# Kernel optimization log

Measured on AMD Instinct MI355X. Metric: run time of the kernel, lower is better.

The kernel has to match this reference:

```python
import jax, jax.numpy as jnp
import numpy as np

# ---------------- static model configuration (mirrors NeuroNN.__init__) -------------
N = 2000
RATIO = 0.8
N_E = int(N * RATIO)
N_I = N - N_E
NMAX = 60          # Euler fixed-point steps (Nmax in Euler2fixedpt)
NAVG = 15          # trailing steps averaged for convergence metric (Navg)
DT = 1e-3
XTOL = 1e-5
XMIN = 1.0
V_THR = 20.0       # spike threshold of Ricciardi transfer fn (V_rest = 0)
SCALING_G = 1.0
W_FF = 30.0
SIG_EXT = 5.0
DEG = jnp.pi / 180.0

_IS_I = jnp.arange(N) >= N_E
PREF = jnp.concatenate([jnp.linspace(0.0, 179.99, N_E), jnp.linspace(0.0, 179.99, N_I)])
T_INV = 1.0 / jnp.where(_IS_I, 0.01 * 0.5, 0.01)          # T_E=0.01, T_I=0.005
TAU = jnp.where(_IS_I, 0.01, 0.01)                          # tau_E = tau_I = 0.01
TAU_REF = jnp.where(_IS_I, 0.001, 0.005)                    # refractory periods
# connection-type gather index: conn[i,j] = 2*(j is I) + (i is I)  -> 0:ee 1:ei 2:ie 3:ii
CONN = 2 * _IS_I[None, :].astype(jnp.int32) + _IS_I[:, None].astype(jnp.int32)
SIGN_COL = jnp.where(_IS_I, -1.0, 1.0)                      # Dale's law: sign by presynaptic column
DIFF = jnp.abs(PREF[:, None] - PREF[None, :])               # |pref_i - pref_j| (deg)

ORIENTATIONS = jnp.arange(12.0) * 15.0                       # [12]
CONTRASTS = jnp.array([0.0, 0.0432773, 0.103411, 0.186966, 0.303066, 0.464386, 0.68854, 1.0])
# circular Gaussian feed-forward drive, [12, N]
_gauss = jnp.exp((jnp.cos(2.0 * DEG * (ORIENTATIONS[:, None] - PREF[None, :])) - 1.0)
                 / (4.0 * (DEG * W_FF) ** 2))
# all 96 conditions flattened: index c*12 + o, shape [96, N]
INPUT_MEAN = (CONTRASTS[:, None, None] * 20.0 * SCALING_G * _gauss[None]).reshape(96, N)

# ------------- Ricciardi transfer function Phi (Sanzeni rational approximation) ------
_A = [0.22757881388024176, 0.77373949685442023, 0.32056016125642045,
      0.32171431660633076, 0.62718906618071668, 0.93524391761244940,
      1.0616084849547165, 0.64290613877355551, 0.14805913578876898]

def f_ricci(x):
    t = -x / (1.0 + x)
    p = jnp.zeros_like(x)
    for c in reversed(_A):      # Horner: a1*t + ... + a9*t^9
        p = p * t + c
    return jnp.log(2.0 * x + 1.0) + p * t

def g_ricci(x):
    z = x / (2.0 + x)
    enum = (3.5441754117462949 * z - 7.0529131065835378 * z**2 - 56.532378057580381 * z**3
            + 279.56761105465944 * z**4 - 520.37554793489681 * z**5
            + 456.58245777026514 * z**6 - 155.73340457809226 * z**7)
    denom = (1.0 - 4.1357968834226053 * z - 7.2984226138266743 * z**2
             + 98.656602235468327 * z**3 - 334.20436223415163 * z**4
             + 601.08633903294185 * z**5 - 599.58577549598340 * z**6
             + 277.18420330693891 * z**7 - 16.445022798669722 * z**8)
    return enum / denom

def Phi(mu, sigma, tau, tau_ref):
    xp = mu / sigma
    xm = (mu - V_THR) / sigma
    pos = xm > 0
    neg = xp <= 0
    mid = (~pos) & (~neg)
    # branch 1: 0 < xm < xp   (guard values keep unselected lanes finite for vjp)
    xps = jnp.where(pos, xp, 2.0)
    xms = jnp.where(pos, xm, 1.0)
    r_pos = 1.0 / (f_ricci(xps) - f_ricci(xms))
    # branch 2: xm <= 0 < xp
    xpm = jnp.where(mid, xp, 1.0)
    nxm = jnp.clip(jnp.where(mid, -xm, 1.0), 0.0, 9.0)
    r_mid = 1.0 / (f_ricci(xpm) + jnp.exp(nxm ** 2) * g_ricci(nxm))
    # branch 3: xm < xp <= 0
    nxp = jnp.clip(jnp.where(neg, -xp, 0.5), 0.0, 9.0)
    nxm2 = jnp.clip(jnp.where(neg, -xm, 1.0), 0.0, 9.0)
    arg = g_ricci(nxm2) - jnp.exp(nxp ** 2 - nxm2 ** 2) * g_ricci(nxp)
    r_neg = jnp.exp(-nxm2 ** 2 - jnp.log(jnp.maximum(arg, 1e-12)))
    r = jnp.where(pos, r_pos, jnp.where(mid, r_mid, r_neg))
    return 1.0 / (tau_ref + tau / jnp.maximum(r, 1e-12))

# --------------------------- weight construction ------------------------------------
def _build_weights(j_param, p_param, w_param, rand_matrix):
    J = jnp.exp(j_param)                         # positive efficacies, [4]
    P = jax.nn.sigmoid(2.0 * jnp.exp(p_param))   # probs in (0,1), steepness-2 sigmoid
    Wd = jnp.exp(w_param)                        # positive widths (deg)
    J_mat = J[CONN]                              # [N, N] gathers by connection type
    P_mat = P[CONN]
    W_mat = Wd[CONN]
    z = jnp.exp((jnp.cos(2.0 * DEG * DIFF) - 1.0) / (4.0 * (DEG * W_mat) ** 2))
    W = SIGN_COL[None, :] * J_mat * jax.nn.sigmoid(32.0 * (P_mat * z - rand_matrix))
    return W, W * W

# ------------------ Euler fixed-point solve, all 96 conditions at once ---------------
def _solve(W, W2):
    sd2 = SIG_EXT ** 2
    def step(r, _):
        mu = TAU * (r @ W.T) + INPUT_MEAN                  # [96, N]
        sig = jnp.sqrt(TAU * (r @ W2.T) + sd2)
        dr = DT * T_INV * (Phi(mu, sig, TAU, TAU_REF) - r)
        r = r + dr
        m = jnp.max(jnp.abs(dr) / jnp.maximum(jnp.abs(r), XMIN), axis=1) / XTOL  # [96]
        return r, m
    r0 = jnp.zeros((96, N), dtype=W.dtype)
    r_fp, ms = jax.lax.scan(step, r0, None, length=NMAX)
    avg_step = jnp.mean(ms[-NAVG:])
    return r_fp, avg_step

def setup_inputs() -> dict:
    key = jax.random.key(0)
    k1, k2, k3, k4 = jax.random.split(key, 4)
    j_param = jnp.log(jnp.array([2.0, 1.5, 3.0, 2.5], dtype=jnp.float32)) + 0.1 * jax.random.normal(k1, (4,), dtype=jnp.float32)
    p_param = jnp.log(jnp.array([0.4, 0.3, 0.5, 0.4], dtype=jnp.float32)) + 0.1 * jax.random.normal(k2, (4,), dtype=jnp.float32)
    w_param = jnp.log(jnp.array([32.0, 32.0, 32.0, 32.0], dtype=jnp.float32)) + 0.1 * jax.random.normal(k3, (4,), dtype=jnp.float32)
    rand_matrix = jax.random.uniform(k4, (N, N), dtype=jnp.float32)
    return {"j_param": j_param, "p_param": p_param, "w_param": w_param, "rand_matrix": rand_matrix}

def reference(j_param, p_param, w_param, rand_matrix):
    W, W2 = _build_weights(j_param, p_param, w_param, rand_matrix)
    r_fp, avg_step = _solve(W, W2)
    # [96, N] -> [8, 12, N] -> [N, contrasts, orientations] (matches permute(2,0,1))
    tuning = r_fp.reshape(8, 12, N).transpose(2, 0, 1)
    return tuning, avg_step
```

## Files before the change

kernel.cpp:

```cpp
#include <hip/hip_runtime.h>
#include <hip/hip_bf16.h>

#define N_NEUR 2000
#define N_E    1600
#define KPAD   2048
#define NCOND  96
#define NSTEP  60
#define NAVG   15
#define NBLK   250
#define RSTEP  (NCOND * KPAD)

#define DEGF   0.017453292519943295f
#define TWO_DEG 0.03490658503988659f

typedef __attribute__((ext_vector_type(8))) short bf16x8;
typedef __attribute__((ext_vector_type(4))) float f32x4;

__device__ __forceinline__ float f_ricci(float x){
    float t = -x / (1.0f + x);
    float p = 0.14805913578876898f;
    p = fmaf(p, t, 0.64290613877355551f);
    p = fmaf(p, t, 1.0616084849547165f);
    p = fmaf(p, t, 0.93524391761244940f);
    p = fmaf(p, t, 0.62718906618071668f);
    p = fmaf(p, t, 0.32171431660633076f);
    p = fmaf(p, t, 0.32056016125642045f);
    p = fmaf(p, t, 0.77373949685442023f);
    p = fmaf(p, t, 0.22757881388024176f);
    return __logf(2.0f * x + 1.0f) + p * t;
}

__device__ __forceinline__ float g_ricci(float x){
    float z = x / (2.0f + x);
    float z2 = z * z, z3 = z2 * z, z4 = z2 * z2, z5 = z4 * z, z6 = z3 * z3, z7 = z6 * z, z8 = z4 * z4;
    float en = 3.5441754117462949f * z - 7.0529131065835378f * z2 - 56.532378057580381f * z3
             + 279.56761105465944f * z4 - 520.37554793489681f * z5
             + 456.58245777026514f * z6 - 155.73340457809226f * z7;
    float de = 1.0f - 4.1357968834226053f * z - 7.2984226138266743f * z2
             + 98.656602235468327f * z3 - 334.20436223415163f * z4
             + 601.08633903294185f * z5 - 599.58577549598340f * z6
             + 277.18420330693891f * z7 - 16.445022798669722f * z8;
    return en / de;
}

__device__ __forceinline__ float phi_rate(float mu, float sigma, float tau_ref){
    const float tau = 0.01f;
    float xp = mu / sigma;
    float xm = (mu - 20.0f) / sigma;
    float r;
    if (xm > 0.0f){
        r = 1.0f / (f_ricci(xp) - f_ricci(xm));
    } else if (xp > 0.0f){
        float nxm = fminf(-xm, 9.0f);
        r = 1.0f / (f_ricci(xp) + __expf(nxm * nxm) * g_ricci(nxm));
    } else {
        float nxp = fminf(fmaxf(-xp, 0.0f), 9.0f);
        float nxm = fminf(-xm, 9.0f);
        float arg = g_ricci(nxm) - __expf(nxp * nxp - nxm * nxm) * g_ricci(nxp);
        r = __expf(-nxm * nxm - __logf(fmaxf(arg, 1e-12f)));
    }
    return 1.0f / (tau_ref + tau / fmaxf(r, 1e-12f));
}

__device__ __forceinline__ float pref_of(int n){
    return (n < N_E) ? (float)n * (179.99f / 1599.0f)
                     : (float)(n - N_E) * (179.99f / 399.0f);
}

__device__ __forceinline__ unsigned short bf16_rne(float f){
    unsigned int u = __float_as_uint(f);
    u = (u + 0x7fffu + ((u >> 16) & 1u)) >> 16;
    return (unsigned short)u;
}

__device__ __forceinline__ void vmdrain(){
    asm volatile("s_waitcnt vmcnt(0)" ::: "memory");
}

__global__ __launch_bounds__(256) void build_w_kernel(
    const float* __restrict__ jp, const float* __restrict__ pp,
    const float* __restrict__ wp, const float* __restrict__ rnd,
    unsigned short* __restrict__ Wh, unsigned short* __restrict__ Wl,
    unsigned short* __restrict__ W2h)
{
    int e = blockIdx.x * 256 + threadIdx.x;
    int i = e >> 11;
    int j = e & (KPAD - 1);
    float w = 0.0f;
    if (i < N_NEUR && j < N_NEUR){
        int isIi = (i >= N_E) ? 1 : 0;
        int isIj = (j >= N_E) ? 1 : 0;
        int conn = 2 * isIj + isIi;
        float J  = expf(jp[conn]);
        float P  = 1.0f / (1.0f + expf(-2.0f * expf(pp[conn])));
        float Wd = expf(wp[conn]);
        float diff = fabsf(pref_of(i) - pref_of(j));
        float dw = DEGF * Wd;
        float z = expf((cosf(TWO_DEG * diff) - 1.0f) / (4.0f * dw * dw));
        float s = 1.0f / (1.0f + expf(-32.0f * (P * z - rnd[i * N_NEUR + j])));
        float sign = isIj ? -1.0f : 1.0f;
        w = sign * J * s;
    }
    unsigned short hb = bf16_rne(w);
    float hf = __uint_as_float(((unsigned int)hb) << 16);
    Wh[e] = hb;
    Wl[e] = bf16_rne(w - hf);
    W2h[e] = bf16_rne(w * w);
}

__global__ __launch_bounds__(256) void build_im_kernel(float* __restrict__ IM)
{
    int e = blockIdx.x * 256 + threadIdx.x;
    int c = e >> 11;
    int n = e & (KPAD - 1);
    if (n >= N_NEUR){ IM[e] = 0.0f; return; }
    const float contrasts[8] = {0.0f, 0.0432773f, 0.103411f, 0.186966f,
                                0.303066f, 0.464386f, 0.68854f, 1.0f};
    int ci = c / 12;
    int oi = c - ci * 12;
    float orient = (float)oi * 15.0f;
    const float dw = DEGF * 30.0f;
    float g = expf((cosf(TWO_DEG * (orient - pref_of(n))) - 1.0f) / (4.0f * dw * dw));
    IM[e] = contrasts[ci] * 20.0f * g;
}

__global__ __launch_bounds__(512, 2) void solve_kernel(
    const unsigned short* __restrict__ Wh, const unsigned short* __restrict__ Wl,
    const unsigned short* __restrict__ W2h,
    unsigned short* __restrict__ rh, unsigned short* __restrict__ rl,
    unsigned int* __restrict__ flags,
    const float* __restrict__ IM, float* __restrict__ out,
    float* __restrict__ mloc)
{
    __shared__ float red[8][64][25];
    __shared__ float vbuf[48][16];

    const int bid  = blockIdx.x;
    const int tile = bid >> 1;
    const int half = bid & 1;
    const int t  = threadIdx.x;
    const int wv = t >> 6;
    const int ln = t & 63;
    const int nbase = tile * 16;
    const int cbase = half * 48;

    const int lrow = ln & 15;
    const int lk8  = (ln >> 4) * 8;
    const int kw   = wv * 256 + lk8;
    const int nrow = nbase + lrow;

    const unsigned short* pwh = &Wh [nrow * KPAD + kw];
    const unsigned short* pwl = &Wl [nrow * KPAD + kw];
    const unsigned short* pw2 = &W2h[nrow * KPAD + kw];
    bf16x8 wh_f[8], wl_f[8], w2_f[8];
    #pragma unroll
    for (int s = 0; s < 8; ++s){
        wh_f[s] = *reinterpret_cast<const bf16x8*>(pwh + s * 32);
        wl_f[s] = *reinterpret_cast<const bf16x8*>(pwl + s * 32);
        w2_f[s] = *reinterpret_cast<const bf16x8*>(pw2 + s * 32);
    }

    const int wt = wv * 16 + (ln & 15);
    const bool need = (ln < 16) && (wt < 125);
    const unsigned int* fpoll = &flags[((size_t)wt * 2 + half) * 16];

    const int o0 = t, o1 = t + 512;
    const bool has1 = (o1 < 768);
    const int c_l0 = o0 >> 4, n_l0 = o0 & 15;
    const int c_l1 = o1 >> 4, n_l1 = o1 & 15;
    const int m0 = c_l0 >> 4, q0 = c_l0 & 3, lr0 = ((c_l0 & 15) >> 2) * 16 + n_l0;
    const int m1 = c_l1 >> 4, q1 = c_l1 & 3, lr1 = ((c_l1 & 15) >> 2) * 16 + n_l1;
    const int c0 = cbase + c_l0, i0n = nbase + n_l0;
    const int c1 = cbase + c_l1, i1n = nbase + n_l1;
    const float im0 = IM[c0 * KPAD + i0n];
    const float im1 = has1 ? IM[c1 * KPAD + i1n] : 0.0f;
    const bool isI0 = (i0n >= N_E), isI1 = (i1n >= N_E);
    float rf0 = 0.0f, rf1 = 0.0f;

    const int ro0 = (cbase + lrow) * KPAD + kw;

    for (int st = 0; st < NSTEP; ++st){
        if (st > 0){
            const unsigned int* fp = fpoll + (size_t)st * 256 * 16;
            for (;;){
                unsigned int v = need ? __hip_atomic_load(fp, __ATOMIC_RELAXED,
                                                          __HIP_MEMORY_SCOPE_AGENT) : 1u;
                if (__all(v != 0)) break;
            }
        }

        const unsigned short* bhp = rh + (size_t)st * RSTEP + ro0;
        const unsigned short* blp = rl + (size_t)st * RSTEP + ro0;

        f32x4 accm[3], accs[3];
        #pragma unroll
        for (int m = 0; m < 3; ++m){
            accm[m] = (f32x4){0.0f, 0.0f, 0.0f, 0.0f};
            accs[m] = (f32x4){0.0f, 0.0f, 0.0f, 0.0f};
        }

        bf16x8 fh[4][3], fl[4][3];
        #define LOADF(b, s) do {                                                        \
            fh[b][0] = *reinterpret_cast<const bf16x8*>(bhp + (s) * 32            );    \
            fh[b][1] = *reinterpret_cast<const bf16x8*>(bhp + (s) * 32 + 16 * KPAD);    \
            fh[b][2] = *reinterpret_cast<const bf16x8*>(bhp + (s) * 32 + 32 * KPAD);    \
            fl[b][0] = *reinterpret_cast<const bf16x8*>(blp + (s) * 32            );    \
            fl[b][1] = *reinterpret_cast<const bf16x8*>(blp + (s) * 32 + 16 * KPAD);    \
            fl[b][2] = *reinterpret_cast<const bf16x8*>(blp + (s) * 32 + 32 * KPAD);    \
        } while (0)

        LOADF(0, 0);
        LOADF(1, 1);
        LOADF(2, 2);
        #pragma unroll
        for (int s = 0; s < 8; ++s){
            const int cur = s & 3;
            if (s + 3 < 8){ const int nx = (s + 3) & 3; LOADF(nx, s + 3); }
            #pragma unroll
            for (int m = 0; m < 3; ++m){
                accm[m] = __builtin_amdgcn_mfma_f32_16x16x32_bf16(fh[cur][m], wh_f[s], accm[m], 0, 0, 0);
                accm[m] = __builtin_amdgcn_mfma_f32_16x16x32_bf16(fh[cur][m], wl_f[s], accm[m], 0, 0, 0);
                accm[m] = __builtin_amdgcn_mfma_f32_16x16x32_bf16(fl[cur][m], wh_f[s], accm[m], 0, 0, 0);
                accs[m] = __builtin_amdgcn_mfma_f32_16x16x32_bf16(fh[cur][m], w2_f[s], accs[m], 0, 0, 0);
                accs[m] = __builtin_amdgcn_mfma_f32_16x16x32_bf16(fl[cur][m], w2_f[s], accs[m], 0, 0, 0);
            }
        }
        #undef LOADF

        #pragma unroll
        for (int m = 0; m < 3; ++m)
            #pragma unroll
            for (int q = 0; q < 4; ++q){
                red[wv][ln][m * 4 + q]      = accm[m][q];
                red[wv][ln][12 + m * 4 + q] = accs[m][q];
            }
        __syncthreads();

        unsigned short* rho = rh + (size_t)(st + 1) * RSTEP;
        unsigned short* rlo = rl + (size_t)(st + 1) * RSTEP;
        const bool track = (st >= NSTEP - NAVG);

        {
            float ms = 0.0f, ss = 0.0f;
            #pragma unroll
            for (int w = 0; w < 8; ++w){
                ms += red[w][lr0][m0 * 4 + q0];
                ss += red[w][lr0][12 + m0 * 4 + q0];
            }
            const float mu = fmaf(0.01f, ms, im0);
            const float sg = sqrtf(fmaf(0.01f, ss, 25.0f));
            const float rate = phi_rate(mu, sg, isI0 ? 0.001f : 0.005f);
            const float dr = (isI0 ? 0.2f : 0.1f) * (rate - rf0);
            const float rnew = rf0 + dr;
            rf0 = rnew;
            const unsigned short hb = bf16_rne(rnew);
            const float hf = __uint_as_float(((unsigned int)hb) << 16);
            __hip_atomic_store(&rho[c0 * KPAD + i0n], hb,
                               __ATOMIC_RELAXED, __HIP_MEMORY_SCOPE_AGENT);
            __hip_atomic_store(&rlo[c0 * KPAD + i0n], bf16_rne(rnew - hf),
                               __ATOMIC_RELAXED, __HIP_MEMORY_SCOPE_AGENT);
            if (track) vbuf[c_l0][n_l0] = fabsf(dr) / fmaxf(fabsf(rnew), 1.0f);
            if (st == NSTEP - 1) out[i0n * NCOND + c0] = rnew;
        }
        if (has1){
            float ms = 0.0f, ss = 0.0f;
            #pragma unroll
            for (int w = 0; w < 8; ++w){
                ms += red[w][lr1][m1 * 4 + q1];
                ss += red[w][lr1][12 + m1 * 4 + q1];
            }
            const float mu = fmaf(0.01f, ms, im1);
            const float sg = sqrtf(fmaf(0.01f, ss, 25.0f));
            const float rate = phi_rate(mu, sg, isI1 ? 0.001f : 0.005f);
            const float dr = (isI1 ? 0.2f : 0.1f) * (rate - rf1);
            const float rnew = rf1 + dr;
            rf1 = rnew;
            const unsigned short hb = bf16_rne(rnew);
            const float hf = __uint_as_float(((unsigned int)hb) << 16);
            __hip_atomic_store(&rho[c1 * KPAD + i1n], hb,
                               __ATOMIC_RELAXED, __HIP_MEMORY_SCOPE_AGENT);
            __hip_atomic_store(&rlo[c1 * KPAD + i1n], bf16_rne(rnew - hf),
                               __ATOMIC_RELAXED, __HIP_MEMORY_SCOPE_AGENT);
            if (track) vbuf[c_l1][n_l1] = fabsf(dr) / fmaxf(fabsf(rnew), 1.0f);
            if (st == NSTEP - 1) out[i1n * NCOND + c1] = rnew;
        }

        vmdrain();
        __syncthreads();
        if (st < NSTEP - 1 && t == 0)
            __hip_atomic_store(&flags[((size_t)(st + 1) * 256 + tile * 2 + half) * 16], 1u,
                               __ATOMIC_RELAXED, __HIP_MEMORY_SCOPE_AGENT);
        if (track && t < 48){
            float mx = 0.0f;
            #pragma unroll
            for (int j = 0; j < 16; ++j) mx = fmaxf(mx, vbuf[t][j]);
            mloc[((size_t)(st - (NSTEP - NAVG)) * NBLK + bid) * 48 + t] = mx;
        }
    }
}

__global__ __launch_bounds__(128) void finalize_max_kernel(
    const float* __restrict__ mloc, float* __restrict__ m2)
{
    int idx = blockIdx.x * 128 + threadIdx.x;
    if (idx >= NAVG * NCOND) return;
    int st = idx / NCOND, c = idx - st * NCOND;
    int half = c / 48, cl = c - half * 48;
    float mx = 0.0f;
    for (int tile = 0; tile < 125; ++tile)
        mx = fmaxf(mx, mloc[((size_t)st * NBLK + tile * 2 + half) * 48 + cl]);
    m2[idx] = mx;
}

__global__ __launch_bounds__(256) void finalize_sum_kernel(
    const float* __restrict__ m2, float* __restrict__ out)
{
    __shared__ float sbuf[256];
    float s = 0.0f;
    for (int i = threadIdx.x; i < NAVG * NCOND; i += 256) s += m2[i];
    sbuf[threadIdx.x] = s;
    __syncthreads();
    for (int st = 128; st > 0; st >>= 1){
        if (threadIdx.x < st) sbuf[threadIdx.x] += sbuf[threadIdx.x + st];
        __syncthreads();
    }
    if (threadIdx.x == 0)
        out[N_NEUR * NCOND] = sbuf[0] / (float)(NAVG * NCOND) * 1e5f;
}

extern "C" void kernel_launch(void* const* d_in, const int* in_sizes, int n_in,
                              void* d_out, int out_size, void* d_ws, size_t ws_size,
                              hipStream_t stream) {
    const float* jp  = (const float*)d_in[0];
    const float* pp  = (const float*)d_in[1];
    const float* wp  = (const float*)d_in[2];
    const float* rnd = (const float*)d_in[3];
    float* out = (float*)d_out;

    const size_t WELEMS = (size_t)KPAD * KPAD;
    const size_t RBUFS  = (size_t)(NSTEP + 1) * RSTEP;
    unsigned short* Wh  = (unsigned short*)d_ws;
    unsigned short* Wl  = Wh  + WELEMS;
    unsigned short* W2h = Wl  + WELEMS;
    float* IM   = (float*)(W2h + WELEMS);
    float* mloc = IM + (size_t)NCOND * KPAD;
    float* m2   = mloc + (size_t)NAVG * NBLK * 48;
    unsigned short* rh = (unsigned short*)(m2 + NAVG * NCOND);
    unsigned short* rl = rh + RBUFS;
    unsigned int* flags = (unsigned int*)(rl + RBUFS);

    hipMemsetAsync(rh, 0, (size_t)RSTEP * sizeof(unsigned short), stream);
    hipMemsetAsync(rl, 0, (size_t)RSTEP * sizeof(unsigned short), stream);
    hipMemsetAsync(flags, 0, (size_t)(NSTEP + 1) * 256 * 16 * sizeof(unsigned int), stream);

    build_w_kernel<<<(int)(WELEMS / 256), 256, 0, stream>>>(jp, pp, wp, rnd, Wh, Wl, W2h);
    build_im_kernel<<<(int)((NCOND * KPAD) / 256), 256, 0, stream>>>(IM);

    solve_kernel<<<dim3(NBLK), dim3(512), 0, stream>>>(
        Wh, Wl, W2h, rh, rl, flags, IM, out, mloc);

    finalize_max_kernel<<<(NAVG * NCOND + 127) / 128, 128, 0, stream>>>(mloc, m2);
    finalize_sum_kernel<<<1, 256, 0, stream>>>(m2, out);
}
```

Baseline: 887.2 us.

## Poll per-slice readiness flags incrementally instead of waiting on all producers upfront

Replaces the single wait for all producer flags at the start of each step with per-slice polling just before each K-slice of the rate vector is loaded. MFMA work on slices that are already published can then overlap with waiting for later producers. The prefetch depth drops from three slices to two, which lowers register pressure but leaves less latency hiding. The finer-grained spin loops also add more polling overhead.

New measurement: 869.9 us, median of 2. Within noise of the previous version (-2.0%).

```diff
diff --git a/kernel.cpp b/kernel.cpp
--- a/kernel.cpp
+++ b/kernel.cpp
@@ -160,9 +160,6 @@
         w2_f[s] = *reinterpret_cast<const bf16x8*>(pw2 + s * 32);
     }
 
-    const int wt = wv * 16 + (ln & 15);
-    const bool need = (ln < 16) && (wt < 125);
-    const unsigned int* fpoll = &flags[((size_t)wt * 2 + half) * 16];
 
     const int o0 = t, o1 = t + 512;
     const bool has1 = (o1 < 768);
@@ -180,15 +177,6 @@
     const int ro0 = (cbase + lrow) * KPAD + kw;
 
     for (int st = 0; st < NSTEP; ++st){
-        if (st > 0){
-            const unsigned int* fp = fpoll + (size_t)st * 256 * 16;
-            for (;;){
-                unsigned int v = need ? __hip_atomic_load(fp, __ATOMIC_RELAXED,
-                                                          __HIP_MEMORY_SCOPE_AGENT) : 1u;
-                if (__all(v != 0)) break;
-            }
-        }
-
         const unsigned short* bhp = rh + (size_t)st * RSTEP + ro0;
         const unsigned short* blp = rl + (size_t)st * RSTEP + ro0;
 
@@ -199,7 +187,22 @@
             accs[m] = (f32x4){0.0f, 0.0f, 0.0f, 0.0f};
         }
 
-        bf16x8 fh[4][3], fl[4][3];
+        #define POLLP(pr) do {                                                          \
+            if (st > 0){                                                                \
+                const int wtp = wv * 16 + 2 * (pr) + ln;                                \
+                const bool needp = (ln < 2) && (wtp < 125);                             \
+                const int wtc = (wtp < 125) ? wtp : 0;                                  \
+                const unsigned int* fpp =                                               \
+                    flags + ((size_t)st * 256 + (size_t)wtc * 2 + half) * 16;           \
+                for (;;){                                                               \
+                    unsigned int vv = needp ? __hip_atomic_load(fpp, __ATOMIC_RELAXED,  \
+                                               __HIP_MEMORY_SCOPE_AGENT) : 1u;          \
+                    if (__all(vv != 0)) break;                                          \
+                }                                                                       \
+            }                                                                           \
+        } while (0)
+
+        bf16x8 fh[3][3], fl[3][3];
         #define LOADF(b, s) do {                                                        \
             fh[b][0] = *reinterpret_cast<const bf16x8*>(bhp + (s) * 32            );    \
             fh[b][1] = *reinterpret_cast<const bf16x8*>(bhp + (s) * 32 + 16 * KPAD);    \
@@ -209,13 +212,16 @@
             fl[b][2] = *reinterpret_cast<const bf16x8*>(blp + (s) * 32 + 32 * KPAD);    \
         } while (0)
 
-        LOADF(0, 0);
-        LOADF(1, 1);
-        LOADF(2, 2);
+        POLLP(0); LOADF(0, 0);
+        POLLP(1); LOADF(1, 1);
         #pragma unroll
         for (int s = 0; s < 8; ++s){
-            const int cur = s & 3;
-            if (s + 3 < 8){ const int nx = (s + 3) & 3; LOADF(nx, s + 3); }
+            const int cur = s % 3;
+            if (s + 2 < 8){
+                const int nx = (s + 2) % 3;
+                POLLP(s + 2);
+                LOADF(nx, s + 2);
+            }
             #pragma unroll
             for (int m = 0; m < 3; ++m){
                 accm[m] = __builtin_amdgcn_mfma_f32_16x16x32_bf16(fh[cur][m], wh_f[s], accm[m], 0, 0, 0);
@@ -226,6 +232,7 @@
             }
         }
         #undef LOADF
+        #undef POLLP
 
         #pragma unroll
         for (int m = 0; m < 3; ++m)
```
